# Kernel tuning notes

Measured on AMD Instinct MI355X. Metric: run time of the kernel, lower is better.

The kernel has to match this reference:

```python
import jax, jax.numpy as jnp
import numpy as np

B, N = 512, 256
NODE_D = 256      # inpt_dim[1]
PE_D = 256        # pooled_edge_dim
GLOB_D = 64       # inpt_dim[2]
FEAT_IN = NODE_D + PE_D          # 512, LN dim
CTXT_IN = GLOB_D                 # ctxt_dim = 0
FEAT_OUT = 256                   # feat_kwargs.outp_dim
N_HEADS = 4                      # attn_kwargs.outp_dim
HEAD_DIM = FEAT_OUT // N_HEADS   # 64
FEAT_HID = 1024
ATTN_HID = 256
LN_EPS = 1e-5


def _mlp(x, w1, b1, w2, b2):
    # DenseNetwork: hidden layer with SiLU, linear output
    h = jax.nn.silu(jnp.einsum('bni,ih->bnh', x, w1) + b1)
    return jnp.einsum('bnh,ho->bno', h, w2) + b2


def setup_inputs() -> dict:
    key = jax.random.key(0)
    ks = jax.random.split(key, 12)
    s = lambda fan_in: 1.0 / np.sqrt(fan_in)
    mask = jax.random.randint(ks[2], (B, N), 0, 2).astype(bool)
    mask = mask.at[:, 0].set(True)  # guarantee >=1 valid node per graph
    return {
        'nodes': jax.random.normal(ks[0], (B, N, NODE_D), jnp.float32),
        'pooled_edges': jax.random.normal(ks[1], (B, N, PE_D), jnp.float32),
        'mask': mask,
        'globs': jax.random.normal(ks[3], (B, GLOB_D), jnp.float32),
        'ln_g': jnp.ones((FEAT_IN,), jnp.float32),
        'ln_b': jnp.zeros((FEAT_IN,), jnp.float32),
        'fw1': jax.random.normal(ks[4], (FEAT_IN + CTXT_IN, FEAT_HID), jnp.float32) * s(FEAT_IN + CTXT_IN),
        'fb1': jnp.zeros((FEAT_HID,), jnp.float32),
        'fw2': jax.random.normal(ks[5], (FEAT_HID, FEAT_OUT), jnp.float32) * s(FEAT_HID),
        'fb2': jnp.zeros((FEAT_OUT,), jnp.float32),
        'aw1': jax.random.normal(ks[6], (FEAT_IN + CTXT_IN, ATTN_HID), jnp.float32) * s(FEAT_IN + CTXT_IN),
        'ab1': jnp.zeros((ATTN_HID,), jnp.float32),
        'aw2': jax.random.normal(ks[7], (ATTN_HID, N_HEADS), jnp.float32) * s(ATTN_HID),
        'ab2': jnp.zeros((N_HEADS,), jnp.float32),
    }


def reference(nodes, pooled_edges, mask, globs, ln_g, ln_b,
              fw1, fb1, fw2, fb2, aw1, ab1, aw2, ab2):
    # concat node feats with pooled edge feats, pre-LN
    x = jnp.concatenate([nodes, pooled_edges], axis=-1)            # [B,N,512]
    mu = jnp.mean(x, axis=-1, keepdims=True)
    var = jnp.mean(jnp.square(x - mu), axis=-1, keepdims=True)
    xn = (x - mu) * jax.lax.rsqrt(var + LN_EPS) * ln_g + ln_b
    # high-level context (globals) broadcast to every node
    ctx = jnp.broadcast_to(globs[:, None, :], (B, N, GLOB_D))
    inp = jnp.concatenate([xn, ctx], axis=-1)                      # [B,N,576]
    # attention pooling weights: pass_with_mask with padval=-inf, softmax over nodes
    scores = _mlp(inp, aw1, ab1, aw2, ab2)                         # [B,N,H]
    scores = jnp.where(mask[..., None], scores, -jnp.inf)
    w = jax.nn.softmax(scores / np.sqrt(FEAT_OUT).astype(np.float32), axis=-2)
    w = jnp.nan_to_num(w)                                          # all-masked graphs -> 0
    pool_w = jnp.repeat(w, HEAD_DIM, axis=-1)                      # [B,N,H*head_dim]
    # feature net: pass_with_mask with padval=0
    feats = _mlp(inp, fw1, fb1, fw2, fb2)                          # [B,N,256]
    feats = jnp.where(mask[..., None], feats, 0.0)
    # additive residual
    new_nodes = feats + nodes
    # attention pooled global
    pooled = jnp.sum(new_nodes * pool_w, axis=-2)                  # [B,256]
    return new_nodes, pooled
```

## Files before the change

### kernel.cpp

```cpp
#include <hip/hip_runtime.h>
#include <cmath>

typedef unsigned short ushort_t;
typedef unsigned char uchar_t;
typedef short short8 __attribute__((ext_vector_type(8)));
typedef float floatx4 __attribute__((ext_vector_type(4)));

#define B_GRAPH 512
#define ROWS 131072
#define IN_D 576
#define FEAT_HID 1024
#define ATTN_HID 256
#define NCAT 1280
#define FEAT_OUT 256
#define BK 32
#define NBUF 3
#define A_TILE (128 * BK)
#define B_TILE (256 * BK)

__device__ __forceinline__ float bf2f(ushort_t h) {
    return __uint_as_float(((unsigned int)h) << 16);
}
__device__ __forceinline__ ushort_t f2bf(float f) {
    unsigned int u = __float_as_uint(f);
    u += 0x7fffu + ((u >> 16) & 1u);
    return (ushort_t)(u >> 16);
}
__device__ __forceinline__ void load4bf(const ushort_t* p, float f[4]) {
    uint2 u = *(const uint2*)p;
    f[0] = __uint_as_float(u.x << 16);
    f[1] = __uint_as_float(u.x & 0xffff0000u);
    f[2] = __uint_as_float(u.y << 16);
    f[3] = __uint_as_float(u.y & 0xffff0000u);
}

__global__ void detect_kernel(const void* nodes, const void* maskp, int* flags) {
    const int t = threadIdx.x;
    const ushort_t* nb = (const ushort_t*)nodes;
    int cnt = 0;
    for (int i = t; i < 4096; i += 256) {
        unsigned e = ((unsigned)nb[i] >> 7) & 0xffu;
        if (e >= 147u) cnt++;
    }
    const unsigned* mw = (const unsigned*)maskp;
    int mcnt = 0;
    for (int i = t; i < 16384; i += 256) {
        if (mw[i] > 1u) mcnt++;
    }
    __shared__ int r1[256], r2[256];
    r1[t] = cnt; r2[t] = mcnt; __syncthreads();
    for (int off = 128; off > 0; off >>= 1) {
        if (t < off) { r1[t] += r1[t + off]; r2[t] += r2[t + off]; }
        __syncthreads();
    }
    if (t == 0) { flags[0] = (r1[0] > 64) ? 1 : 0; flags[1] = (r2[0] > 16) ? 1 : 0; }
}

__device__ __forceinline__ float loadany(const void* p, size_t i, int flag) {
    return flag ? ((const float*)p)[i] : bf2f(((const ushort_t*)p)[i]);
}
__device__ __forceinline__ bool maskany(const void* p, size_t i, int flagM) {
    return flagM ? (((const uchar_t*)p)[i] != 0) : (((const int*)p)[i] != 0);
}

__global__ __launch_bounds__(256)
void convert_all(const void* globs, const void* lng, const void* lnb,
                 const void* fb1, const void* fb2, const void* ab1, const void* ab2,
                 ushort_t* gcan, ushort_t* lgc, ushort_t* lbc,
                 ushort_t* bcat, ushort_t* fb2c, ushort_t* ab2c,
                 const int* flags) {
    const int flag = flags[0];
    int i = blockIdx.x * 256 + threadIdx.x;
    if (i < 32768) { gcan[i] = f2bf(loadany(globs, i, flag)); return; }
    i -= 32768;
    if (i < 512)   { lgc[i]  = f2bf(loadany(lng,   i, flag)); return; }
    i -= 512;
    if (i < 512)   { lbc[i]  = f2bf(loadany(lnb,   i, flag)); return; }
    i -= 512;
    if (i < 1024)  { bcat[i] = f2bf(loadany(fb1,   i, flag)); return; }
    i -= 1024;
    if (i < 256)   { bcat[1024 + i] = f2bf(loadany(ab1, i, flag)); return; }
    i -= 256;
    if (i < 256)   { fb2c[i] = f2bf(loadany(fb2,   i, flag)); return; }
    i -= 256;
    if (i < 4)     { ab2c[i] = f2bf(loadany(ab2,   i, flag)); }
}

__global__ __launch_bounds__(256)
void transpose_all(const void* fw1, const void* fw2, const void* aw1, const void* aw2,
                   ushort_t* w1cat, ushort_t* fw2t, ushort_t* aw2t,
                   const int* flags) {
    const int flag = flags[0];
    int i = blockIdx.x * 256 + threadIdx.x;
    if (i < 576 * 1024) {
        int r = i >> 10, c = i & 1023;
        w1cat[(size_t)c * 576 + r] = f2bf(loadany(fw1, i, flag)); return;
    }
    i -= 576 * 1024;
    if (i < 1024 * 256) {
        int r = i >> 8, c = i & 255;
        fw2t[(size_t)c * 1024 + r] = f2bf(loadany(fw2, i, flag)); return;
    }
    i -= 1024 * 256;
    if (i < 576 * 256) {
        int r = i >> 8, c = i & 255;
        w1cat[(size_t)(1024 + c) * 576 + r] = f2bf(loadany(aw1, i, flag)); return;
    }
    i -= 576 * 256;
    if (i < 256 * 4) {
        int r = i >> 2, c = i & 3;
        aw2t[(size_t)c * 256 + r] = f2bf(loadany(aw2, i, flag));
    }
}

__global__ __launch_bounds__(256)
void ln_concat_kernel(const void* __restrict__ nodes, const void* __restrict__ pe,
                      const ushort_t* __restrict__ gcan,
                      const ushort_t* __restrict__ lg, const ushort_t* __restrict__ lb,
                      ushort_t* __restrict__ inp, int row0, const int* __restrict__ flags) {
    const int flag = flags[0];
    const int row  = blockIdx.x * 4 + (threadIdx.x >> 6);
    const int lane = threadIdx.x & 63;
    const size_t grow = (size_t)row0 + row;
    float xa[4], xb[4];
    if (flag) {
        float4 a = *(const float4*)((const float*)nodes + grow * 256 + lane * 4);
        float4 b = *(const float4*)((const float*)pe    + grow * 256 + lane * 4);
        xa[0]=a.x; xa[1]=a.y; xa[2]=a.z; xa[3]=a.w;
        xb[0]=b.x; xb[1]=b.y; xb[2]=b.z; xb[3]=b.w;
    } else {
        load4bf((const ushort_t*)nodes + grow * 256 + lane * 4, xa);
        load4bf((const ushort_t*)pe    + grow * 256 + lane * 4, xb);
    }
    float s = 0.f, q = 0.f;
#pragma unroll
    for (int j = 0; j < 4; j++) { s += xa[j] + xb[j]; q += xa[j]*xa[j] + xb[j]*xb[j]; }
#pragma unroll
    for (int m = 1; m < 64; m <<= 1) { s += __shfl_xor(s, m, 64); q += __shfl_xor(q, m, 64); }
    const float mu   = s * (1.0f / 512.0f);
    const float var  = q * (1.0f / 512.0f) - mu * mu;
    const float rstd = rsqrtf(fmaxf(var, 0.f) + 1e-5f);
    float ga[4], gb[4], ba[4], bb[4];
    load4bf(lg + lane * 4, ga);  load4bf(lg + 256 + lane * 4, gb);
    load4bf(lb + lane * 4, ba);  load4bf(lb + 256 + lane * 4, bb);
    ushort_t r0[4], r1[4];
#pragma unroll
    for (int j = 0; j < 4; j++) {
        r0[j] = f2bf((xa[j] - mu) * rstd * ga[j] + ba[j]);
        r1[j] = f2bf((xb[j] - mu) * rstd * gb[j] + bb[j]);
    }
    ushort_t* op = inp + (size_t)row * IN_D;
    uint2 p0, p1;
    p0.x = (unsigned)r0[0] | ((unsigned)r0[1] << 16);
    p0.y = (unsigned)r0[2] | ((unsigned)r0[3] << 16);
    p1.x = (unsigned)r1[0] | ((unsigned)r1[1] << 16);
    p1.y = (unsigned)r1[2] | ((unsigned)r1[3] << 16);
    *(uint2*)(op + lane * 4)       = p0;
    *(uint2*)(op + 256 + lane * 4) = p1;
    op[512 + lane] = gcan[(grow >> 8) * 64 + lane];
}

struct GemmCore {
    floatx4 acc[8][4];
    int wn, r16, quad;
};

__device__ __forceinline__ void gload16(const ushort_t* g, ushort_t* l) {
    __builtin_amdgcn_global_load_lds(
        (const __attribute__((address_space(1))) unsigned int*)g,
        (__attribute__((address_space(3))) unsigned int*)l, 16, 0, 0);
}
__device__ __forceinline__ unsigned lds_off(const void* p) {
    return (unsigned)(size_t)(const __attribute__((address_space(3))) char*)p;
}

__device__ __forceinline__ void gemm_core(GemmCore& g,
        const ushort_t* __restrict__ A, int lda, const ushort_t* __restrict__ Bt,
        int m0, int n0, int K, ushort_t* As, ushort_t* Bs) {
    const int tid = threadIdx.x;
    const int wave = tid >> 6, lane = tid & 63;
    g.wn = wave * 64; g.r16 = lane & 15; g.quad = lane >> 4;
#pragma unroll
    for (int i = 0; i < 8; i++)
#pragma unroll
        for (int j = 0; j < 4; j++) g.acc[i][j] = (floatx4){0.f, 0.f, 0.f, 0.f};

    const int sr   = lane >> 2;
    const int scol = (lane & 3) * 8;
    const ushort_t* Ag = A  + (size_t)(m0 + wave * 32 + sr) * lda + scol;
    const ushort_t* Bg = Bt + (size_t)(n0 + wave * 64 + sr) * K  + scol;
    ushort_t* Asw = As + wave * 32 * BK;
    ushort_t* Bsw = Bs + wave * 64 * BK;

    const unsigned a_lane = lds_off(As) + (unsigned)((g.r16 * BK + g.quad * 8) * 2);
    const unsigned b_lane = lds_off(Bs) + (unsigned)(((g.wn + g.r16) * BK + g.quad * 8) * 2);

    const int NT = K / BK;
#define STAGE_TILE(T, BUF) do {                                        \
        const size_t kb = (size_t)(T) * BK;                            \
        ushort_t* Ad = Asw + (BUF) * A_TILE;                           \
        ushort_t* Bd = Bsw + (BUF) * B_TILE;                           \
        gload16(Ag + kb,                    Ad);                       \
        gload16(Ag + kb + 16 * (size_t)lda, Ad + 16 * BK);             \
        gload16(Bg + kb,                    Bd);                       \
        gload16(Bg + kb + 16 * (size_t)K,   Bd + 16 * BK);             \
        gload16(Bg + kb + 32 * (size_t)K,   Bd + 32 * BK);             \
        gload16(Bg + kb + 48 * (size_t)K,   Bd + 48 * BK);             \
    } while (0)

    STAGE_TILE(0, 0);
    if (NT > 1) STAGE_TILE(1, 1);

    int bufc = 0;
    for (int t = 0; t < NT; ++t) {
        if (t + 1 < NT) asm volatile("s_waitcnt vmcnt(6)" ::: "memory");
        else            asm volatile("s_waitcnt vmcnt(0)" ::: "memory");
        __builtin_amdgcn_s_barrier();
        __builtin_amdgcn_sched_barrier(0);
        if (t + 2 < NT) {
            int bn = bufc + 2; if (bn >= NBUF) bn -= NBUF;
            STAGE_TILE(t + 2, bn);
        }
        const unsigned aaddr = a_lane + (unsigned)(bufc * (A_TILE * 2));
        const unsigned baddr = b_lane + (unsigned)(bufc * (B_TILE * 2));
        short8 af[8], bg[4];
#pragma unroll
        for (int i = 0; i < 8; i++)
            asm volatile("ds_read_b128 %0, %1 offset:%c2"
                         : "=v"(af[i]) : "v"(aaddr), "i"(i * 1024));
#pragma unroll
        for (int i = 0; i < 4; i++)
            asm volatile("ds_read_b128 %0, %1 offset:%c2"
                         : "=v"(bg[i]) : "v"(baddr), "i"(i * 1024));
        asm volatile("s_waitcnt lgkmcnt(0)" ::: "memory");
        __builtin_amdgcn_sched_barrier(0);
#pragma unroll
        for (int mi = 0; mi < 8; mi++)
#pragma unroll
            for (int ni = 0; ni < 4; ni++)
                g.acc[mi][ni] = __builtin_amdgcn_mfma_f32_16x16x32_bf16(
                    af[mi], bg[ni], g.acc[mi][ni], 0, 0, 0);
        bufc = bufc + 1 == NBUF ? 0 : bufc + 1;
    }
#undef STAGE_TILE
}

__global__ __launch_bounds__(256, 2)
void gemm_silu(const ushort_t* __restrict__ A, int lda,
               const ushort_t* __restrict__ Bt,
               const ushort_t* __restrict__ bias, ushort_t* __restrict__ out,
               int N, int K) {
    __shared__ __align__(16) ushort_t As[NBUF * A_TILE];
    __shared__ __align__(16) ushort_t Bs[NBUF * B_TILE];
    const int m0 = blockIdx.x * 128, n0 = blockIdx.y * 256;
    GemmCore g;
    gemm_core(g, A, lda, Bt, m0, n0, K, As, Bs);
#pragma unroll
    for (int mi = 0; mi < 8; mi++) {
        const int rbase = m0 + mi * 16 + g.quad * 4;
#pragma unroll
        for (int ni = 0; ni < 4; ni++) {
            const int col = n0 + g.wn + ni * 16 + g.r16;
            const float bv = bf2f(bias[col]);
#pragma unroll
            for (int r = 0; r < 4; r++) {
                float v = g.acc[mi][ni][r] + bv;
                v = v / (1.0f + expf(-v));
                out[(size_t)(rbase + r) * N + col] = f2bf(v);
            }
        }
    }
}

__global__ __launch_bounds__(256, 2)
void gemm_out(const ushort_t* __restrict__ A, int lda,
              const ushort_t* __restrict__ Bt,
              const ushort_t* __restrict__ bias, void* __restrict__ out,
              const void* __restrict__ mask, const void* __restrict__ resid,
              int row0, int K, const int* __restrict__ flags) {
    __shared__ __align__(16) ushort_t As[NBUF * A_TILE];
    __shared__ __align__(16) ushort_t Bs[NBUF * B_TILE];
    const int flag = flags[0], flagM = flags[1];
    const int m0 = blockIdx.x * 128, n0 = blockIdx.y * 256;
    GemmCore g;
    gemm_core(g, A, lda, Bt, m0, n0, K, As, Bs);
#pragma unroll
    for (int mi = 0; mi < 8; mi++) {
        const int rbase = m0 + mi * 16 + g.quad * 4;
#pragma unroll
        for (int ni = 0; ni < 4; ni++) {
            const int col = n0 + g.wn + ni * 16 + g.r16;
            const float bv = bf2f(bias[col]);
#pragma unroll
            for (int r = 0; r < 4; r++) {
                const size_t grow = (size_t)row0 + rbase + r;
                const float nd = loadany(resid, grow * FEAT_OUT + col, flag);
                const bool mk = maskany(mask, grow, flagM);
                float v = mk ? (g.acc[mi][ni][r] + bv + nd) : nd;
                if (flag) ((float*)out)[grow * FEAT_OUT + col] = v;
                else      ((ushort_t*)out)[grow * FEAT_OUT + col] = f2bf(v);
            }
        }
    }
}

__global__ __launch_bounds__(256)
void scores_kernel(const ushort_t* __restrict__ hcat,
                   const ushort_t* __restrict__ aw2t,
                   const ushort_t* __restrict__ ab2c,
                   float* __restrict__ scores, int row0) {
    const int row  = blockIdx.x * 4 + (threadIdx.x >> 6);
    const int lane = threadIdx.x & 63;
    float x[4];
    load4bf(hcat + (size_t)row * NCAT + 1024 + lane * 4, x);
    float acc[4];
#pragma unroll
    for (int h = 0; h < 4; h++) {
        float wv[4];
        load4bf(aw2t + h * 256 + lane * 4, wv);
        acc[h] = x[0]*wv[0] + x[1]*wv[1] + x[2]*wv[2] + x[3]*wv[3];
    }
#pragma unroll
    for (int m = 1; m < 64; m <<= 1)
#pragma unroll
        for (int h = 0; h < 4; h++) acc[h] += __shfl_xor(acc[h], m, 64);
    if (lane == 0) {
#pragma unroll
        for (int h = 0; h < 4; h++)
            scores[((size_t)row0 + row) * 4 + h] = acc[h] + bf2f(ab2c[h]);
    }
}

__global__ __launch_bounds__(256)
void softmax_kernel(const float* __restrict__ scores, const void* __restrict__ mask,
                    float* __restrict__ w, const int* __restrict__ flags) {
    const int flagM = flags[1];
    const int b = blockIdx.x, n = threadIdx.x;
    const int idx = b * 256 + n;
    float4 s = *(const float4*)(scores + (size_t)idx * 4);
    s.x *= 0.0625f; s.y *= 0.0625f; s.z *= 0.0625f; s.w *= 0.0625f;
    const bool mk = maskany(mask, idx, flagM);
    __shared__ float4 red[256];
    float4 v;
    v.x = mk ? s.x : -3.0e38f; v.y = mk ? s.y : -3.0e38f;
    v.z = mk ? s.z : -3.0e38f; v.w = mk ? s.w : -3.0e38f;
    red[n] = v; __syncthreads();
    for (int off = 128; off > 0; off >>= 1) {
        if (n < off) {
            float4 o = red[n + off], c = red[n];
            c.x = fmaxf(c.x, o.x); c.y = fmaxf(c.y, o.y);
            c.z = fmaxf(c.z, o.z); c.w = fmaxf(c.w, o.w);
            red[n] = c;
        }
        __syncthreads();
    }
    float4 mx = red[0]; __syncthreads();
    float4 e;
    e.x = mk ? expf(s.x - mx.x) : 0.f; e.y = mk ? expf(s.y - mx.y) : 0.f;
    e.z = mk ? expf(s.z - mx.z) : 0.f; e.w = mk ? expf(s.w - mx.w) : 0.f;
    red[n] = e; __syncthreads();
    for (int off = 128; off > 0; off >>= 1) {
        if (n < off) {
            float4 o = red[n + off], c = red[n];
            c.x += o.x; c.y += o.y; c.z += o.z; c.w += o.w;
            red[n] = c;
        }
        __syncthreads();
    }
    float4 sm = red[0];
    const float ix = (sm.x > 0.f) ? 1.f / sm.x : 0.f;
    const float iy = (sm.y > 0.f) ? 1.f / sm.y : 0.f;
    const float iz = (sm.z > 0.f) ? 1.f / sm.z : 0.f;
    const float iw = (sm.w > 0.f) ? 1.f / sm.w : 0.f;
    float4 r; r.x = e.x * ix; r.y = e.y * iy; r.z = e.z * iz; r.w = e.w * iw;
    *(float4*)(w + (size_t)idx * 4) = r;
}

__global__ __launch_bounds__(256)
void pooled_kernel(const void* __restrict__ dout, const float* __restrict__ w,
                   const int* __restrict__ flags) {
    const int flag = flags[0];
    const int b = blockIdx.x, t = threadIdx.x;
    __shared__ float wsh[1024];
    const float* wb = w + (size_t)b * 1024;
    for (int i = t; i < 1024; i += 256) wsh[i] = wb[i];
    __syncthreads();
    const int h = t >> 6;
    float acc = 0.f;
    const size_t base = (size_t)b * 65536;
    if (flag) {
        const float* nn = (const float*)dout + base;
#pragma unroll 4
        for (int n = 0; n < 256; n++) acc += nn[(size_t)n * 256 + t] * wsh[n * 4 + h];
        ((float*)dout)[(size_t)ROWS * 256 + (size_t)b * 256 + t] = acc;
    } else {
        const ushort_t* nn = (const ushort_t*)dout + base;
#pragma unroll 4
        for (int n = 0; n < 256; n++) acc += bf2f(nn[(size_t)n * 256 + t]) * wsh[n * 4 + h];
        ((ushort_t*)dout)[(size_t)ROWS * 256 + (size_t)b * 256 + t] = f2bf(acc);
    }
}

extern "C" void kernel_launch(void* const* d_in, const int* in_sizes, int n_in,
                              void* d_out, int out_size, void* d_ws, size_t ws_size,
                              hipStream_t stream) {
    (void)in_sizes; (void)n_in; (void)out_size;
    const void* nodes = d_in[0];
    const void* pe    = d_in[1];
    const void* mask  = d_in[2];
    const void* globs = d_in[3];
    const void* ln_g  = d_in[4];
    const void* ln_b  = d_in[5];
    const void* fw1   = d_in[6];
    const void* fb1   = d_in[7];
    const void* fw2   = d_in[8];
    const void* fb2   = d_in[9];
    const void* aw1   = d_in[10];
    const void* ab1   = d_in[11];
    const void* aw2   = d_in[12];
    const void* ab2   = d_in[13];

    int CHR;
    if      (ws_size >= (size_t)140 * 1024 * 1024) CHR = 32768;
    else if (ws_size >= (size_t)80  * 1024 * 1024) CHR = 16384;
    else                                           CHR = 8192;

    char* ws = (char*)d_ws;
    size_t o = 0;
    auto take = [&](size_t bytes) -> char* {
        char* p = ws + o;
        o += (bytes + 255) & ~(size_t)255;
        return p;
    };
    ushort_t* inp  = (ushort_t*)take((size_t)CHR * IN_D * 2);
    ushort_t* hcat = (ushort_t*)take((size_t)CHR * NCAT * 2);
    float*    sc   = (float*)   take((size_t)ROWS * 4 * 4);
    float*    wsm  = (float*)   take((size_t)ROWS * 4 * 4);
    ushort_t* w1cat= (ushort_t*)take((size_t)NCAT * 576 * 2);
    ushort_t* fw2t = (ushort_t*)take(1024 * 256 * 2);
    ushort_t* aw2t = (ushort_t*)take(256 * 4 * 2);
    ushort_t* gcan = (ushort_t*)take(32768 * 2);
    ushort_t* lgc  = (ushort_t*)take(512 * 2);
    ushort_t* lbc  = (ushort_t*)take(512 * 2);
    ushort_t* bcat = (ushort_t*)take((size_t)NCAT * 2);
    ushort_t* fb2c = (ushort_t*)take(256 * 2);
    ushort_t* ab2c = (ushort_t*)take(4 * 2);
    int*      flags= (int*)     take(64);

    detect_kernel<<<1, 256, 0, stream>>>(nodes, mask, flags);
    convert_all<<<139, 256, 0, stream>>>(globs, ln_g, ln_b, fb1, fb2, ab1, ab2,
                                         gcan, lgc, lbc, bcat, fb2c, ab2c, flags);
    transpose_all<<<3908, 256, 0, stream>>>(fw1, fw2, aw1, aw2,
                                            w1cat, fw2t, aw2t, flags);

    const int nchunk = ROWS / CHR;
    for (int c = 0; c < nchunk; c++) {
        const int row0 = c * CHR;
        ln_concat_kernel<<<CHR / 4, 256, 0, stream>>>(nodes, pe, gcan, lgc, lbc,
                                                      inp, row0, flags);
        gemm_silu<<<dim3(CHR / 128, NCAT / 256), 256, 0, stream>>>(
            inp, IN_D, w1cat, bcat, hcat, NCAT, IN_D);
        scores_kernel<<<CHR / 4, 256, 0, stream>>>(hcat, aw2t, ab2c, sc, row0);
        gemm_out<<<dim3(CHR / 128, FEAT_OUT / 256), 256, 0, stream>>>(
            hcat, NCAT, fw2t, fb2c, d_out, mask, nodes, row0, FEAT_HID, flags);
    }

    softmax_kernel<<<B_GRAPH, 256, 0, stream>>>(sc, mask, wsm, flags);
    pooled_kernel<<<B_GRAPH, 256, 0, stream>>>(d_out, wsm, flags);
}
```

Before: 968.0 us.

## Swap MFMA operands for row-contiguous epilogue stores and halve gemm_out M-tile

The MFMA operand order is swapped so each lane holds four consecutive output columns of one row. This lets the SiLU and residual epilogues do vectorized bias loads, packed bf16 conversion and wide stores instead of scattered 2-byte stores. gemm_out is templated to a 64-row tile, doubling its block count to improve occupancy and CU coverage for the narrow N=256 output GEMM, with the vmcnt wait adjusted to match. SiLU now uses fast exp and reciprocal, which is slightly less precise.

```diff
diff --git a/kernel.cpp b/kernel.cpp
--- a/kernel.cpp
+++ b/kernel.cpp
@@ -15,8 +15,6 @@
 #define FEAT_OUT 256
 #define BK 32
 #define NBUF 3
-#define A_TILE (128 * BK)
-#define B_TILE (256 * BK)
 
 __device__ __forceinline__ float bf2f(ushort_t h) {
     return __uint_as_float(((unsigned int)h) << 16);
@@ -32,6 +30,15 @@
     f[1] = __uint_as_float(u.x & 0xffff0000u);
     f[2] = __uint_as_float(u.y << 16);
     f[3] = __uint_as_float(u.y & 0xffff0000u);
+}
+__device__ __forceinline__ unsigned cvtpk_bf16(float lo, float hi) {
+    unsigned r;
+    asm("v_cvt_pk_bf16_f32 %0, %1, %2" : "=v"(r) : "v"(lo), "v"(hi));
+    return r;
+}
+__device__ __forceinline__ float silu_fast(float v) {
+    const float e = __expf(-v);
+    return v * __builtin_amdgcn_rcpf(1.0f + e);
 }
 
 __global__ void detect_kernel(const void* nodes, const void* maskp, int* flags) {
@@ -160,8 +167,9 @@
     op[512 + lane] = gcan[(grow >> 8) * 64 + lane];
 }
 
+template <int MI>
 struct GemmCore {
-    floatx4 acc[8][4];
+    floatx4 acc[MI][4];
     int wn, r16, quad;
 };
 
@@ -174,38 +182,45 @@
     return (unsigned)(size_t)(const __attribute__((address_space(3))) char*)p;
 }
 
-__device__ __forceinline__ void gemm_core(GemmCore& g,
+template <int MI>
+__device__ __forceinline__ void gemm_core(GemmCore<MI>& g,
         const ushort_t* __restrict__ A, int lda, const ushort_t* __restrict__ Bt,
         int m0, int n0, int K, ushort_t* As, ushort_t* Bs) {
+    constexpr int AROWS = MI * 16;
+    constexpr int A_T   = AROWS * BK;
+    constexpr int B_T   = 256 * BK;
+    constexpr int ARW   = AROWS / 4;
+    constexpr int LPT   = AROWS / 64 + 4;
     const int tid = threadIdx.x;
     const int wave = tid >> 6, lane = tid & 63;
     g.wn = wave * 64; g.r16 = lane & 15; g.quad = lane >> 4;
 #pragma unroll
-    for (int i = 0; i < 8; i++)
+    for (int i = 0; i < MI; i++)
 #pragma unroll
         for (int j = 0; j < 4; j++) g.acc[i][j] = (floatx4){0.f, 0.f, 0.f, 0.f};
 
     const int sr   = lane >> 2;
     const int scol = (lane & 3) * 8;
-    const ushort_t* Ag = A  + (size_t)(m0 + wave * 32 + sr) * lda + scol;
+    const ushort_t* Ag = A  + (size_t)(m0 + wave * ARW + sr) * lda + scol;
     const ushort_t* Bg = Bt + (size_t)(n0 + wave * 64 + sr) * K  + scol;
-    ushort_t* Asw = As + wave * 32 * BK;
+    ushort_t* Asw = As + wave * ARW * BK;
     ushort_t* Bsw = Bs + wave * 64 * BK;
 
     const unsigned a_lane = lds_off(As) + (unsigned)((g.r16 * BK + g.quad * 8) * 2);
     const unsigned b_lane = lds_off(Bs) + (unsigned)(((g.wn + g.r16) * BK + g.quad * 8) * 2);
 
     const int NT = K / BK;
-#define STAGE_TILE(T, BUF) do {                                        \
-        const size_t kb = (size_t)(T) * BK;                            \
-        ushort_t* Ad = Asw + (BUF) * A_TILE;                           \
-        ushort_t* Bd = Bsw + (BUF) * B_TILE;                           \
-        gload16(Ag + kb,                    Ad);                       \
-        gload16(Ag + kb + 16 * (size_t)lda, Ad + 16 * BK);             \
-        gload16(Bg + kb,                    Bd);                       \
-        gload16(Bg + kb + 16 * (size_t)K,   Bd + 16 * BK);             \
-        gload16(Bg + kb + 32 * (size_t)K,   Bd + 32 * BK);             \
-        gload16(Bg + kb + 48 * (size_t)K,   Bd + 48 * BK);             \
+#define STAGE_TILE(T, BUF) do {                                          \
+        const size_t kb = (size_t)(T) * BK;                              \
+        ushort_t* Ad = Asw + (BUF) * A_T;                                \
+        ushort_t* Bd = Bsw + (BUF) * B_T;                                \
+        gload16(Ag + kb, Ad);                                            \
+        if constexpr (AROWS == 128)                                      \
+            gload16(Ag + kb + 16 * (size_t)lda, Ad + 16 * BK);           \
+        gload16(Bg + kb,                    Bd);                         \
+        gload16(Bg + kb + 16 * (size_t)K,   Bd + 16 * BK);               \
+        gload16(Bg + kb + 32 * (size_t)K,   Bd + 32 * BK);               \
+        gload16(Bg + kb + 48 * (size_t)K,   Bd + 48 * BK);               \
     } while (0)
 
     STAGE_TILE(0, 0);
@@ -213,19 +228,23 @@
 
     int bufc = 0;
     for (int t = 0; t < NT; ++t) {
-        if (t + 1 < NT) asm volatile("s_waitcnt vmcnt(6)" ::: "memory");
-        else            asm volatile("s_waitcnt vmcnt(0)" ::: "memory");
+        if (t + 1 < NT) {
+            if constexpr (LPT == 6) asm volatile("s_waitcnt vmcnt(6)" ::: "memory");
+            else                    asm volatile("s_waitcnt vmcnt(5)" ::: "memory");
+        } else {
+            asm volatile("s_waitcnt vmcnt(0)" ::: "memory");
+        }
         __builtin_amdgcn_s_barrier();
         __builtin_amdgcn_sched_barrier(0);
         if (t + 2 < NT) {
             int bn = bufc + 2; if (bn >= NBUF) bn -= NBUF;
             STAGE_TILE(t + 2, bn);
         }
-        const unsigned aaddr = a_lane + (unsigned)(bufc * (A_TILE * 2));
-        const unsigned baddr = b_lane + (unsigned)(bufc * (B_TILE * 2));
-        short8 af[8], bg[4];
-#pragma unroll
-        for (int i = 0; i < 8; i++)
+        const unsigned aaddr = a_lane + (unsigned)(bufc * (A_T * 2));
+        const unsigned baddr = b_lane + (unsigned)(bufc * (B_T * 2));
+        short8 af[MI], bg[4];
+#pragma unroll
+        for (int i = 0; i < MI; i++)
             asm volatile("ds_read_b128 %0, %1 offset:%c2"
                          : "=v"(af[i]) : "v"(aaddr), "i"(i * 1024));
 #pragma unroll
@@ -235,11 +254,11 @@
         asm volatile("s_waitcnt lgkmcnt(0)" ::: "memory");
         __builtin_amdgcn_sched_barrier(0);
 #pragma unroll
-        for (int mi = 0; mi < 8; mi++)
+        for (int mi = 0; mi < MI; mi++)
 #pragma unroll
             for (int ni = 0; ni < 4; ni++)
                 g.acc[mi][ni] = __builtin_amdgcn_mfma_f32_16x16x32_bf16(
-                    af[mi], bg[ni], g.acc[mi][ni], 0, 0, 0);
+                    bg[ni], af[mi], g.acc[mi][ni], 0, 0, 0);
         bufc = bufc + 1 == NBUF ? 0 : bufc + 1;
     }
 #undef STAGE_TILE
@@ -250,24 +269,29 @@
                const ushort_t* __restrict__ Bt,
                const ushort_t* __restrict__ bias, ushort_t* __restrict__ out,
                int N, int K) {
-    __shared__ __align__(16) ushort_t As[NBUF * A_TILE];
-    __shared__ __align__(16) ushort_t Bs[NBUF * B_TILE];
+    __shared__ __align__(16) ushort_t As[NBUF * 128 * BK];
+    __shared__ __align__(16) ushort_t Bs[NBUF * 256 * BK];
     const int m0 = blockIdx.x * 128, n0 = blockIdx.y * 256;
-    GemmCore g;
-    gemm_core(g, A, lda, Bt, m0, n0, K, As, Bs);
+    GemmCore<8> g;
+    gemm_core<8>(g, A, lda, Bt, m0, n0, K, As, Bs);
+    float bv[4][4];
+#pragma unroll
+    for (int ni = 0; ni < 4; ni++)
+        load4bf(bias + n0 + g.wn + ni * 16 + g.quad * 4, bv[ni]);
 #pragma unroll
     for (int mi = 0; mi < 8; mi++) {
-        const int rbase = m0 + mi * 16 + g.quad * 4;
+        const int row = m0 + mi * 16 + g.r16;
+        ushort_t* orow = out + (size_t)row * N + n0 + g.wn + g.quad * 4;
 #pragma unroll
         for (int ni = 0; ni < 4; ni++) {
-            const int col = n0 + g.wn + ni * 16 + g.r16;
-            const float bv = bf2f(bias[col]);
-#pragma unroll
-            for (int r = 0; r < 4; r++) {
-                float v = g.acc[mi][ni][r] + bv;
-                v = v / (1.0f + expf(-v));
-                out[(size_t)(rbase + r) * N + col] = f2bf(v);
-            }
+            float v[4];
+#pragma unroll
+            for (int r = 0; r < 4; r++)
+                v[r] = silu_fast(g.acc[mi][ni][r] + bv[ni][r]);
+            uint2 p;
+            p.x = cvtpk_bf16(v[0], v[1]);
+            p.y = cvtpk_bf16(v[2], v[3]);
+            *(uint2*)(orow + ni * 16) = p;
         }
     }
 }
@@ -278,27 +302,49 @@
               const ushort_t* __restrict__ bias, void* __restrict__ out,
               const void* __restrict__ mask, const void* __restrict__ resid,
               int row0, int K, const int* __restrict__ flags) {
-    __shared__ __align__(16) ushort_t As[NBUF * A_TILE];
-    __shared__ __align__(16) ushort_t Bs[NBUF * B_TILE];
+    __shared__ __align__(16) ushort_t As[NBUF * 64 * BK];
+    __shared__ __align__(16) ushort_t Bs[NBUF * 256 * BK];
     const int flag = flags[0], flagM = flags[1];
-    const int m0 = blockIdx.x * 128, n0 = blockIdx.y * 256;
-    GemmCore g;
-    gemm_core(g, A, lda, Bt, m0, n0, K, As, Bs);
-#pragma unroll
-    for (int mi = 0; mi < 8; mi++) {
-        const int rbase = m0 + mi * 16 + g.quad * 4;
-#pragma unroll
-        for (int ni = 0; ni < 4; ni++) {
-            const int col = n0 + g.wn + ni * 16 + g.r16;
-            const float bv = bf2f(bias[col]);
-#pragma unroll
-            for (int r = 0; r < 4; r++) {
-                const size_t grow = (size_t)row0 + rbase + r;
-                const float nd = loadany(resid, grow * FEAT_OUT + col, flag);
-                const bool mk = maskany(mask, grow, flagM);
-                float v = mk ? (g.acc[mi][ni][r] + bv + nd) : nd;
-                if (flag) ((float*)out)[grow * FEAT_OUT + col] = v;
-                else      ((ushort_t*)out)[grow * FEAT_OUT + col] = f2bf(v);
+    const int m0 = blockIdx.x * 64;
+    GemmCore<4> g;
+    gemm_core<4>(g, A, lda, Bt, m0, 0, K, As, Bs);
+    float bv[4][4];
+#pragma unroll
+    for (int ni = 0; ni < 4; ni++)
+        load4bf(bias + g.wn + ni * 16 + g.quad * 4, bv[ni]);
+#pragma unroll
+    for (int mi = 0; mi < 4; mi++) {
+        const size_t grow = (size_t)row0 + m0 + mi * 16 + g.r16;
+        const bool mk = maskany(mask, grow, flagM);
+        const size_t cbase = grow * FEAT_OUT + g.wn + g.quad * 4;
+        if (flag) {
+            const float* rrow = (const float*)resid + cbase;
+            float* orow = (float*)out + cbase;
+#pragma unroll
+            for (int ni = 0; ni < 4; ni++) {
+                float4 nd = *(const float4*)(rrow + ni * 16);
+                float4 o;
+                o.x = mk ? (g.acc[mi][ni][0] + bv[ni][0] + nd.x) : nd.x;
+                o.y = mk ? (g.acc[mi][ni][1] + bv[ni][1] + nd.y) : nd.y;
+                o.z = mk ? (g.acc[mi][ni][2] + bv[ni][2] + nd.z) : nd.z;
+                o.w = mk ? (g.acc[mi][ni][3] + bv[ni][3] + nd.w) : nd.w;
+                *(float4*)(orow + ni * 16) = o;
+            }
+        } else {
+            const ushort_t* rrow = (const ushort_t*)resid + cbase;
+            ushort_t* orow = (ushort_t*)out + cbase;
+#pragma unroll
+            for (int ni = 0; ni < 4; ni++) {
+                float nd[4];
+                load4bf(rrow + ni * 16, nd);
+                float v[4];
+#pragma unroll
+                for (int r = 0; r < 4; r++)
+                    v[r] = mk ? (g.acc[mi][ni][r] + bv[ni][r] + nd[r]) : nd[r];
+                uint2 p;
+                p.x = cvtpk_bf16(v[0], v[1]);
+                p.y = cvtpk_bf16(v[2], v[3]);
+                *(uint2*)(orow + ni * 16) = p;
             }
         }
     }
@@ -461,7 +507,7 @@
         gemm_silu<<<dim3(CHR / 128, NCAT / 256), 256, 0, stream>>>(
             inp, IN_D, w1cat, bcat, hcat, NCAT, IN_D);
         scores_kernel<<<CHR / 4, 256, 0, stream>>>(hcat, aw2t, ab2c, sc, row0);
-        gemm_out<<<dim3(CHR / 128, FEAT_OUT / 256), 256, 0, stream>>>(
+        gemm_out<<<dim3(CHR / 64, 1), 256, 0, stream>>>(
             hcat, NCAT, fw2t, fb2c, d_out, mask, nodes, row0, FEAT_HID, flags);
     }
 
```

After: 869.3 us. -10.2%, faster.
